# Optimization experiments

Hardware: AMD Instinct MI355X
Metric: run time of the kernel (lower is better)

Reference implementation:

```python
import jax, jax.numpy as jnp
import numpy as np

M = 0.5
S = 64.0
LS_EPS = 0.0
COS_M = float(np.cos(M))
SIN_M = float(np.sin(M))
THRESHOLD = float(np.cos(np.pi - M))
MM = float(np.sin(np.pi - M) * M)
N_CLASSES = 100000


def setup_inputs() -> dict:
    key = jax.random.key(0)
    k1, k2, k3 = jax.random.split(key, 3)
    embeddings = jax.random.normal(k1, (1024, 512), dtype=jnp.float32)
    kernel = jax.random.normal(k2, (512, N_CLASSES), dtype=jnp.float32) * 0.01
    t = jnp.zeros((1,), dtype=jnp.float32)
    label = jax.random.randint(k3, (1024,), 0, N_CLASSES, dtype=jnp.int64)
    return {"embeddings": embeddings, "kernel": kernel, "t": t, "label": label}


def reference(embeddings, kernel, t, label):
    # l2-normalize embeddings over feature axis, kernel over input axis
    emb = embeddings / jnp.linalg.norm(embeddings, axis=1, keepdims=True)
    kn = kernel / jnp.linalg.norm(kernel, axis=0, keepdims=True)
    cos_theta = jnp.clip(emb @ kn, -1.0, 1.0)  # [N, C]
    n = embeddings.shape[0]
    rows = jnp.arange(n)
    target_logit = cos_theta[rows, label][:, None]  # [N, 1]
    sin_theta = jnp.sqrt(1.0 - target_logit ** 2)
    cos_theta_m = target_logit * COS_M - sin_theta * SIN_M  # [N, 1]
    mask = cos_theta > cos_theta_m  # hard examples (broadcast per row)
    final_target_logit = jnp.where(target_logit > THRESHOLD,
                                   cos_theta_m, target_logit - MM)
    # running-mean buffer update (no-grad in original)
    t_new = jax.lax.stop_gradient(target_logit.mean() * 0.01 + 0.99 * t[0])
    cos_theta = jnp.where(mask, cos_theta * (t_new + cos_theta), cos_theta)
    cos_theta = cos_theta.at[rows, label].set(final_target_logit[:, 0])
    if LS_EPS > 0:
        cos_theta = (1 - LS_EPS) * cos_theta + LS_EPS / N_CLASSES
    return cos_theta * S
```

## Files before the change

### kernel.cpp

```cpp
#include <hip/hip_runtime.h>

typedef unsigned short u16;
typedef unsigned int u32;
typedef __attribute__((ext_vector_type(8))) short bf16x8;
typedef __attribute__((ext_vector_type(4))) float f32x4;

#define KDIM   512
#define NROWS  1024
#define NCLS   100000
#define CPAD   100096
#define NSTRIP 782
#define NMT    8

#define COS_M_C   0.8775825618903728f
#define SIN_M_C   0.4794255386042030f
#define THRESH_C  (-0.8775825618903728f)
#define MM_C      0.2397127693021015f
#define S_C       64.0f

__device__ __forceinline__ u16 f2bf(float f) {
    u32 x = __float_as_uint(f);
    x += 0x7fffu + ((x >> 16) & 1u);
    return (u16)(x >> 16);
}
__device__ __forceinline__ float bf2f(u16 u) {
    return __uint_as_float(((u32)u) << 16);
}
__device__ __forceinline__ u32 pack2(float a, float b) {
    return (u32)f2bf(a) | ((u32)f2bf(b) << 16);
}
__device__ __forceinline__ int phi(int r, int q) {
    return r * 4 + ((q + r + (r >> 1)) & 3);
}

__device__ __forceinline__ void gld16(const void* g, void* l) {
    __builtin_amdgcn_global_load_lds(
        (const __attribute__((address_space(1))) void*)g,
        (__attribute__((address_space(3))) void*)l, 16, 0, 0);
}

__global__ __launch_bounds__(64)
void norm_emb_k(const float* __restrict__ emb, float* __restrict__ Af,
                u16* __restrict__ Aw) {
    const int i = blockIdx.x, l = threadIdx.x;
    const float* e = emb + i * KDIM;
    float4 v0 = *(const float4*)(e + l * 8);
    float4 v1 = *(const float4*)(e + l * 8 + 4);
    float s = v0.x*v0.x + v0.y*v0.y + v0.z*v0.z + v0.w*v0.w
            + v1.x*v1.x + v1.y*v1.y + v1.z*v1.z + v1.w*v1.w;
    #pragma unroll
    for (int o = 1; o < 64; o <<= 1) s += __shfl_xor(s, o);
    float inv = rsqrtf(s);
    float4 n0 = make_float4(v0.x*inv, v0.y*inv, v0.z*inv, v0.w*inv);
    float4 n1 = make_float4(v1.x*inv, v1.y*inv, v1.z*inv, v1.w*inv);
    *(float4*)(Af + i*KDIM + l*8)     = n0;
    *(float4*)(Af + i*KDIM + l*8 + 4) = n1;
    const int mt = i >> 7, g = (i >> 4) & 7, r = i & 15;
    const int kc = l >> 2, q = l & 3;
    uint4 w;
    w.x = pack2(n0.x, n0.y);
    w.y = pack2(n0.z, n0.w);
    w.z = pack2(n1.x, n1.y);
    w.w = pack2(n1.z, n1.w);
    *(uint4*)(Aw + mt*65536 + kc*4096 + g*512 + phi(r, q)*8) = w;
}

__global__ __launch_bounds__(128)
void transpose_norm_k(const float* __restrict__ Kg, u16* __restrict__ Bn,
                      float* __restrict__ kinv) {
    __shared__ float Ls[32 * 132];
    const int t  = threadIdx.x;
    const int jb = blockIdx.x * 128;
    const int j  = jb + t;
    u16* bstrip = Bn + (size_t)blockIdx.x * 65536;
    float acc = 0.f;
    for (int kc = 0; kc < 16; ++kc) {
        #pragma unroll
        for (int it = 0; it < 8; ++it) {
            int fid  = it * 128 + t;
            int r    = fid >> 5;
            int c4   = (fid & 31) * 4;
            int gcol = jb + c4;
            float4 v;
            if (gcol + 3 < NCLS) {
                v = *(const float4*)(Kg + (kc*32 + r) * NCLS + gcol);
            } else {
                v.x = (gcol + 0 < NCLS) ? Kg[(kc*32 + r)*NCLS + gcol + 0] : 0.f;
                v.y = (gcol + 1 < NCLS) ? Kg[(kc*32 + r)*NCLS + gcol + 1] : 0.f;
                v.z = (gcol + 2 < NCLS) ? Kg[(kc*32 + r)*NCLS + gcol + 2] : 0.f;
                v.w = (gcol + 3 < NCLS) ? Kg[(kc*32 + r)*NCLS + gcol + 3] : 0.f;
            }
            *(float4*)(Ls + r * 132 + c4) = v;
        }
        __syncthreads();
        #pragma unroll
        for (int q = 0; q < 4; ++q) {
            u16 u[8];
            #pragma unroll
            for (int e = 0; e < 8; ++e) {
                float v = Ls[(q*8 + e) * 132 + t];
                acc += v * v;
                u[e] = f2bf(v);
            }
            uint4 w;
            w.x = (u32)u[0] | ((u32)u[1] << 16);
            w.y = (u32)u[2] | ((u32)u[3] << 16);
            w.z = (u32)u[4] | ((u32)u[5] << 16);
            w.w = (u32)u[6] | ((u32)u[7] << 16);
            *(uint4*)(bstrip + kc*4096 + (t>>4)*512 + phi(t & 15, q)*8) = w;
        }
        __syncthreads();
    }
    kinv[j] = rsqrtf(fmaxf(acc, 1e-30f));
}

__global__ __launch_bounds__(64)
void target_k(const float* __restrict__ Af, const u16* __restrict__ Bn,
              const float* __restrict__ kinv, const int* __restrict__ label,
              float* __restrict__ tgt, float* __restrict__ ctm,
              float* __restrict__ fin) {
    const int i = blockIdx.x, l = threadIdx.x;
    const int lab = label[i];
    const float* a = Af + i * KDIM + l * 8;
    float4 a0 = *(const float4*)a;
    float4 a1 = *(const float4*)(a + 4);
    uint4 bv = *(const uint4*)(Bn + (size_t)(lab >> 7) * 65536
               + (l >> 2) * 4096 + ((lab >> 4) & 7) * 512 + phi(lab & 15, l & 3) * 8);
    float d = a0.x * bf2f((u16)(bv.x & 0xffff)) + a0.y * bf2f((u16)(bv.x >> 16))
            + a0.z * bf2f((u16)(bv.y & 0xffff)) + a0.w * bf2f((u16)(bv.y >> 16))
            + a1.x * bf2f((u16)(bv.z & 0xffff)) + a1.y * bf2f((u16)(bv.z >> 16))
            + a1.z * bf2f((u16)(bv.w & 0xffff)) + a1.w * bf2f((u16)(bv.w >> 16));
    #pragma unroll
    for (int o = 1; o < 64; o <<= 1) d += __shfl_xor(d, o);
    if (l == 0) {
        float c = d * kinv[lab];
        c = fminf(fmaxf(c, -1.f), 1.f);
        tgt[i] = c;
        float sn = sqrtf(fmaxf(1.f - c*c, 0.f));
        float cm = c * COS_M_C - sn * SIN_M_C;
        ctm[i] = cm;
        fin[i] = (c > THRESH_C) ? cm : (c - MM_C);
    }
}

__global__ __launch_bounds__(256)
void tnew_k(const float* __restrict__ tgt, const float* __restrict__ tin,
            float* __restrict__ tnw) {
    __shared__ float red[256];
    const int t = threadIdx.x;
    float s = tgt[t] + tgt[t + 256] + tgt[t + 512] + tgt[t + 768];
    red[t] = s;
    __syncthreads();
    for (int o = 128; o > 0; o >>= 1) {
        if (t < o) red[t] += red[t + o];
        __syncthreads();
    }
    if (t == 0) tnw[0] = red[0] * (0.01f / 1024.f) + 0.99f * tin[0];
}

__global__ __launch_bounds__(256, 4)
void gemm_k(const u16* __restrict__ A, const u16* __restrict__ B,
            const float* __restrict__ kinv, const float* __restrict__ ctm,
            const float* __restrict__ fin, const int* __restrict__ label,
            const float* __restrict__ tnwp, float* __restrict__ out) {
    __shared__ __align__(16) u16 As[2][4096];
    __shared__ __align__(16) u16 Bs[2][4096];
    const int tid  = threadIdx.x;
    const int wave = tid >> 6, lane = tid & 63;

    const int L  = blockIdx.x;
    const int w  = (L & 7) * NSTRIP + (L >> 3);
    const int mt = w & 7;
    const int cs = w >> 3;
    const int m0 = mt * 128;
    const int j0 = cs * 128;
    const int wr = (wave >> 1) * 64;
    const int wc = (wave & 1) * 64;

    f32x4 acc[4][4] = {};

    const u16* gA = A + mt * 65536 + tid * 8;
    const u16* gB = B + (size_t)cs * 65536 + tid * 8;
    const int l0 = tid * 8, l1 = tid * 8 + 2048;

    const int pphi = phi(lane & 15, lane >> 4) * 16;
    const int aG = (wr >> 4) * 1024 + pphi;
    const int bG = (wc >> 4) * 1024 + pphi;

#define STAGE(b, ks) do {                               \
    gld16(gA + (ks) * 4096,        &As[b][l0]);         \
    gld16(gA + (ks) * 4096 + 2048, &As[b][l1]);         \
    gld16(gB + (ks) * 4096,        &Bs[b][l0]);         \
    gld16(gB + (ks) * 4096 + 2048, &Bs[b][l1]);         \
} while (0)

    STAGE(0, 0);
    STAGE(1, 1);
    #pragma unroll
    for (int ks = 0; ks < 16; ++ks) {
        const int cur = ks & 1;
        if (ks < 15) asm volatile("s_waitcnt vmcnt(4)" ::: "memory");
        else         asm volatile("s_waitcnt vmcnt(0)" ::: "memory");
        __builtin_amdgcn_s_barrier();
        __builtin_amdgcn_sched_barrier(0);

        const char* ab = (const char*)As[cur] + aG;
        const char* bb = (const char*)Bs[cur] + bG;
        bf16x8 af[4], bfr[4];
        #pragma unroll
        for (int m = 0; m < 4; ++m)
            af[m] = *(const bf16x8*)(ab + m * 1024);
        #pragma unroll
        for (int n = 0; n < 4; ++n)
            bfr[n] = *(const bf16x8*)(bb + n * 1024);

        asm volatile("s_waitcnt lgkmcnt(0)" ::: "memory");
        __builtin_amdgcn_sched_barrier(0);
        __builtin_amdgcn_s_barrier();
        __builtin_amdgcn_sched_barrier(0);

        if (ks < 14) STAGE(cur, ks + 2);

        __builtin_amdgcn_s_setprio(1);
        #pragma unroll
        for (int m = 0; m < 4; ++m)
            #pragma unroll
            for (int n = 0; n < 4; ++n)
                acc[m][n] = __builtin_amdgcn_mfma_f32_16x16x32_bf16(
                                af[m], bfr[n], acc[m][n], 0, 0, 0);
        __builtin_amdgcn_s_setprio(0);
    }
#undef STAGE

    const float tnew = *tnwp;
    const int colbase = j0 + wc + (lane & 15);
    float kv[4];
    int cols[4];
    #pragma unroll
    for (int n = 0; n < 4; ++n) {
        cols[n] = colbase + n * 16;
        kv[n] = (cols[n] < NCLS) ? kinv[cols[n]] : 0.f;
    }
    #pragma unroll
    for (int m = 0; m < 4; ++m) {
        const int rb = m0 + wr + m * 16 + (lane >> 4) * 4;
        #pragma unroll
        for (int r = 0; r < 4; ++r) {
            const int row = rb + r;
            const int lab = label[row];
            const float ct = ctm[row];
            const float fv = fin[row];
            float* orow = out + (size_t)row * NCLS;
            #pragma unroll
            for (int n = 0; n < 4; ++n) {
                float c = acc[m][n][r] * kv[n];
                c = fminf(fmaxf(c, -1.f), 1.f);
                float v = (c > ct) ? c * (tnew + c) : c;
                v = (cols[n] == lab) ? fv : v;
                if (cols[n] < NCLS)
                    orow[cols[n]] = v * S_C;
            }
        }
    }
}

extern "C" void kernel_launch(void* const* d_in, const int* in_sizes, int n_in,
                              void* d_out, int out_size, void* d_ws, size_t ws_size,
                              hipStream_t stream) {
    const float* emb = (const float*)d_in[0];
    const float* Kg  = (const float*)d_in[1];
    const float* tin = (const float*)d_in[2];
    const int*   lab = (const int*)d_in[3];
    float* out = (float*)d_out;

    char* w = (char*)d_ws;
    u16*   Bn   = (u16*)w;
    u16*   Aw   = (u16*)(w + 102498304);
    float* Af   = (float*)(w + 103546880);
    float* kinv = (float*)(w + 105644032);
    float* tgt  = (float*)(w + 106044416);
    float* ctmv = (float*)(w + 106048512);
    float* finv = (float*)(w + 106052608);
    float* tnw  = (float*)(w + 106056704);

    norm_emb_k<<<NROWS, 64, 0, stream>>>(emb, Af, Aw);
    transpose_norm_k<<<NSTRIP, 128, 0, stream>>>(Kg, Bn, kinv);
    target_k<<<NROWS, 64, 0, stream>>>(Af, Bn, kinv, lab, tgt, ctmv, finv);
    tnew_k<<<1, 256, 0, stream>>>(tgt, tin, tnw);
    gemm_k<<<NSTRIP * NMT, 256, 0, stream>>>(
        Aw, Bn, kinv, ctmv, finv, lab, tnw, out);
}
```

Before: 370.0 us.

## Enlarge GEMM tile to 256x256 with 512 threads and XOR-swizzled 64-K layout

The GEMM block tile grows from 128x128 with 256 threads to 256x256 with 512 threads. Each wave now computes 128x64, and the K step is 64, so there are 8 iterations instead of 16. The packed A/B layouts in the normalization and transpose kernels switch to a row-major 64-wide K chunk with an XOR-style swizzle. The pipeline also prefetches the next stage before waiting, and the XCD-aware block remap is adjusted. The goal is more data reuse per byte loaded and fewer barriers. The cost is higher register and LDS use, 64 KB per block, and lower occupancy.

After: 388.3 us. +4.9%, slower.

```diff
diff --git a/kernel.cpp b/kernel.cpp
--- a/kernel.cpp
+++ b/kernel.cpp
@@ -9,8 +9,9 @@
 #define NROWS  1024
 #define NCLS   100000
 #define CPAD   100096
-#define NSTRIP 782
-#define NMT    8
+#define NSTRIP 391
+#define NMT    4
+#define NWG    (NSTRIP*NMT)
 
 #define COS_M_C   0.8775825618903728f
 #define SIN_M_C   0.4794255386042030f
@@ -29,15 +30,13 @@
 __device__ __forceinline__ u32 pack2(float a, float b) {
     return (u32)f2bf(a) | ((u32)f2bf(b) << 16);
 }
-__device__ __forceinline__ int phi(int r, int q) {
-    return r * 4 + ((q + r + (r >> 1)) & 3);
-}
 
 __device__ __forceinline__ void gld16(const void* g, void* l) {
     __builtin_amdgcn_global_load_lds(
         (const __attribute__((address_space(1))) void*)g,
         (__attribute__((address_space(3))) void*)l, 16, 0, 0);
 }
+
 
 __global__ __launch_bounds__(64)
 void norm_emb_k(const float* __restrict__ emb, float* __restrict__ Af,
@@ -55,31 +54,31 @@
     float4 n1 = make_float4(v1.x*inv, v1.y*inv, v1.z*inv, v1.w*inv);
     *(float4*)(Af + i*KDIM + l*8)     = n0;
     *(float4*)(Af + i*KDIM + l*8 + 4) = n1;
-    const int mt = i >> 7, g = (i >> 4) & 7, r = i & 15;
-    const int kc = l >> 2, q = l & 3;
+    const int mt = i >> 8, row = i & 255;
     uint4 w;
     w.x = pack2(n0.x, n0.y);
     w.y = pack2(n0.z, n0.w);
     w.z = pack2(n1.x, n1.y);
     w.w = pack2(n1.z, n1.w);
-    *(uint4*)(Aw + mt*65536 + kc*4096 + g*512 + phi(r, q)*8) = w;
-}
-
-__global__ __launch_bounds__(128)
+    *(uint4*)(Aw + mt*131072 + (l>>3)*16384 + row*64
+              + (((l&7) + row) & 7) * 8) = w;
+}
+
+__global__ __launch_bounds__(256)
 void transpose_norm_k(const float* __restrict__ Kg, u16* __restrict__ Bn,
                       float* __restrict__ kinv) {
-    __shared__ float Ls[32 * 132];
+    __shared__ float Ls[32 * 260];
     const int t  = threadIdx.x;
-    const int jb = blockIdx.x * 128;
+    const int jb = blockIdx.x * 256;
     const int j  = jb + t;
-    u16* bstrip = Bn + (size_t)blockIdx.x * 65536;
+    u16* bstrip = Bn + (size_t)blockIdx.x * 131072;
     float acc = 0.f;
     for (int kc = 0; kc < 16; ++kc) {
         #pragma unroll
         for (int it = 0; it < 8; ++it) {
-            int fid  = it * 128 + t;
-            int r    = fid >> 5;
-            int c4   = (fid & 31) * 4;
+            int fid  = it * 256 + t;
+            int r    = fid >> 6;
+            int c4   = (fid & 63) * 4;
             int gcol = jb + c4;
             float4 v;
             if (gcol + 3 < NCLS) {
@@ -90,15 +89,15 @@
                 v.z = (gcol + 2 < NCLS) ? Kg[(kc*32 + r)*NCLS + gcol + 2] : 0.f;
                 v.w = (gcol + 3 < NCLS) ? Kg[(kc*32 + r)*NCLS + gcol + 3] : 0.f;
             }
-            *(float4*)(Ls + r * 132 + c4) = v;
+            *(float4*)(Ls + r * 260 + c4) = v;
         }
         __syncthreads();
         #pragma unroll
-        for (int q = 0; q < 4; ++q) {
+        for (int sub = 0; sub < 4; ++sub) {
             u16 u[8];
             #pragma unroll
             for (int e = 0; e < 8; ++e) {
-                float v = Ls[(q*8 + e) * 132 + t];
+                float v = Ls[(sub*8 + e) * 260 + t];
                 acc += v * v;
                 u[e] = f2bf(v);
             }
@@ -107,7 +106,8 @@
             w.y = (u32)u[2] | ((u32)u[3] << 16);
             w.z = (u32)u[4] | ((u32)u[5] << 16);
             w.w = (u32)u[6] | ((u32)u[7] << 16);
-            *(uint4*)(bstrip + kc*4096 + (t>>4)*512 + phi(t & 15, q)*8) = w;
+            *(uint4*)(bstrip + (kc>>1)*16384 + t*64
+                      + ((((kc&1)*4 + sub) + t) & 7) * 8) = w;
         }
         __syncthreads();
     }
@@ -121,11 +121,12 @@
               float* __restrict__ fin) {
     const int i = blockIdx.x, l = threadIdx.x;
     const int lab = label[i];
-    const float* a = Af + i * KDIM + l * 8;
-    float4 a0 = *(const float4*)a;
-    float4 a1 = *(const float4*)(a + 4);
-    uint4 bv = *(const uint4*)(Bn + (size_t)(lab >> 7) * 65536
-               + (l >> 2) * 4096 + ((lab >> 4) & 7) * 512 + phi(lab & 15, l & 3) * 8);
+    const int kbase = (l >> 3) * 64 + (l & 7) * 8;
+    float4 a0 = *(const float4*)(Af + i * KDIM + kbase);
+    float4 a1 = *(const float4*)(Af + i * KDIM + kbase + 4);
+    const int col = lab & 255;
+    uint4 bv = *(const uint4*)(Bn + (size_t)(lab >> 8) * 131072
+               + (l >> 3) * 16384 + col * 64 + (((l & 7) + col) & 7) * 8);
     float d = a0.x * bf2f((u16)(bv.x & 0xffff)) + a0.y * bf2f((u16)(bv.x >> 16))
             + a0.z * bf2f((u16)(bv.y & 0xffff)) + a0.w * bf2f((u16)(bv.y >> 16))
             + a1.x * bf2f((u16)(bv.z & 0xffff)) + a1.y * bf2f((u16)(bv.z >> 16))
@@ -158,92 +159,118 @@
     if (t == 0) tnw[0] = red[0] * (0.01f / 1024.f) + 0.99f * tin[0];
 }
 
-__global__ __launch_bounds__(256, 4)
+__global__ __launch_bounds__(512, 2)
 void gemm_k(const u16* __restrict__ A, const u16* __restrict__ B,
             const float* __restrict__ kinv, const float* __restrict__ ctm,
             const float* __restrict__ fin, const int* __restrict__ label,
             const float* __restrict__ tnwp, float* __restrict__ out) {
-    __shared__ __align__(16) u16 As[2][4096];
-    __shared__ __align__(16) u16 Bs[2][4096];
+    __shared__ __align__(16) u16 As[2][16384];
+    __shared__ __align__(16) u16 Bs[2][16384];
     const int tid  = threadIdx.x;
     const int wave = tid >> 6, lane = tid & 63;
 
-    const int L  = blockIdx.x;
-    const int w  = (L & 7) * NSTRIP + (L >> 3);
-    const int mt = w & 7;
-    const int cs = w >> 3;
-    const int m0 = mt * 128;
-    const int j0 = cs * 128;
-    const int wr = (wave >> 1) * 64;
-    const int wc = (wave & 1) * 64;
-
-    f32x4 acc[4][4] = {};
-
-    const u16* gA = A + mt * 65536 + tid * 8;
-    const u16* gB = B + (size_t)cs * 65536 + tid * 8;
-    const int l0 = tid * 8, l1 = tid * 8 + 2048;
-
-    const int pphi = phi(lane & 15, lane >> 4) * 16;
-    const int aG = (wr >> 4) * 1024 + pphi;
-    const int bG = (wc >> 4) * 1024 + pphi;
-
-#define STAGE(b, ks) do {                               \
-    gld16(gA + (ks) * 4096,        &As[b][l0]);         \
-    gld16(gA + (ks) * 4096 + 2048, &As[b][l1]);         \
-    gld16(gB + (ks) * 4096,        &Bs[b][l0]);         \
-    gld16(gB + (ks) * 4096 + 2048, &Bs[b][l1]);         \
+    const int L   = blockIdx.x;
+    const int xcd = L & 7;
+    const int wg  = (xcd < 4 ? xcd * 196 : 784 + (xcd - 4) * 195) + (L >> 3);
+    const int mt  = wg & 3;
+    const int cs  = wg >> 2;
+    const int m0  = mt * 256;
+    const int j0  = cs * 256;
+    const int wrl = (wave >> 2) * 128;
+    const int wcl = (wave & 3) * 64;
+
+    f32x4 acc[8][4] = {};
+
+    const u16* gA = A + mt * 131072 + tid * 8;
+    const u16* gB = B + (size_t)cs * 131072 + tid * 8;
+    const int  ld = tid * 8;
+
+    const int rowA = wrl + (lane & 15);
+    const int colB = wcl + (lane & 15);
+    const int qh   = lane >> 4;
+    const int aOff0 = rowA * 64 + ((qh     + rowA) & 7) * 8;
+    const int aOff1 = rowA * 64 + ((qh + 4 + rowA) & 7) * 8;
+    const int bOff0 = colB * 64 + ((qh     + colB) & 7) * 8;
+    const int bOff1 = colB * 64 + ((qh + 4 + colB) & 7) * 8;
+
+#define STAGE(b, kt) do {                                        \
+    gld16(gA + (kt)*16384 +     0, &As[b][ld]);                  \
+    gld16(gA + (kt)*16384 +  4096, &As[b][ld + 4096]);           \
+    gld16(gA + (kt)*16384 +  8192, &As[b][ld + 8192]);           \
+    gld16(gA + (kt)*16384 + 12288, &As[b][ld + 12288]);          \
+    gld16(gB + (kt)*16384 +     0, &Bs[b][ld]);                  \
+    gld16(gB + (kt)*16384 +  4096, &Bs[b][ld + 4096]);           \
+    gld16(gB + (kt)*16384 +  8192, &Bs[b][ld + 8192]);           \
+    gld16(gB + (kt)*16384 + 12288, &Bs[b][ld + 12288]);          \
 } while (0)
 
     STAGE(0, 0);
-    STAGE(1, 1);
-    #pragma unroll
-    for (int ks = 0; ks < 16; ++ks) {
-        const int cur = ks & 1;
-        if (ks < 15) asm volatile("s_waitcnt vmcnt(4)" ::: "memory");
-        else         asm volatile("s_waitcnt vmcnt(0)" ::: "memory");
+    #pragma unroll 2
+    for (int kt = 0; kt < 8; ++kt) {
+        const int cur = kt & 1;
+        if (kt < 7) {
+            STAGE(cur ^ 1, kt + 1);
+            asm volatile("s_waitcnt vmcnt(8)" ::: "memory");
+        } else {
+            asm volatile("s_waitcnt vmcnt(0)" ::: "memory");
+        }
         __builtin_amdgcn_s_barrier();
         __builtin_amdgcn_sched_barrier(0);
 
-        const char* ab = (const char*)As[cur] + aG;
-        const char* bb = (const char*)Bs[cur] + bG;
-        bf16x8 af[4], bfr[4];
-        #pragma unroll
-        for (int m = 0; m < 4; ++m)
-            af[m] = *(const bf16x8*)(ab + m * 1024);
+        const u16* a = As[cur];
+        const u16* b = Bs[cur];
+        bf16x8 af[8], bfr[4];
+
+        #pragma unroll
+        for (int m = 0; m < 8; ++m)
+            af[m] = *(const bf16x8*)(a + aOff0 + m * 1024);
         #pragma unroll
         for (int n = 0; n < 4; ++n)
-            bfr[n] = *(const bf16x8*)(bb + n * 1024);
-
+            bfr[n] = *(const bf16x8*)(b + bOff0 + n * 1024);
         asm volatile("s_waitcnt lgkmcnt(0)" ::: "memory");
         __builtin_amdgcn_sched_barrier(0);
-        __builtin_amdgcn_s_barrier();
-        __builtin_amdgcn_sched_barrier(0);
-
-        if (ks < 14) STAGE(cur, ks + 2);
-
         __builtin_amdgcn_s_setprio(1);
         #pragma unroll
-        for (int m = 0; m < 4; ++m)
+        for (int m = 0; m < 8; ++m)
             #pragma unroll
             for (int n = 0; n < 4; ++n)
                 acc[m][n] = __builtin_amdgcn_mfma_f32_16x16x32_bf16(
                                 af[m], bfr[n], acc[m][n], 0, 0, 0);
         __builtin_amdgcn_s_setprio(0);
+
+        #pragma unroll
+        for (int m = 0; m < 8; ++m)
+            af[m] = *(const bf16x8*)(a + aOff1 + m * 1024);
+        #pragma unroll
+        for (int n = 0; n < 4; ++n)
+            bfr[n] = *(const bf16x8*)(b + bOff1 + n * 1024);
+        asm volatile("s_waitcnt lgkmcnt(0)" ::: "memory");
+        __builtin_amdgcn_sched_barrier(0);
+        __builtin_amdgcn_s_barrier();
+        __builtin_amdgcn_sched_barrier(0);
+        __builtin_amdgcn_s_setprio(1);
+        #pragma unroll
+        for (int m = 0; m < 8; ++m)
+            #pragma unroll
+            for (int n = 0; n < 4; ++n)
+                acc[m][n] = __builtin_amdgcn_mfma_f32_16x16x32_bf16(
+                                af[m], bfr[n], acc[m][n], 0, 0, 0);
+        __builtin_amdgcn_s_setprio(0);
     }
 #undef STAGE
 
     const float tnew = *tnwp;
-    const int colbase = j0 + wc + (lane & 15);
+    const int colbase = j0 + wcl + (lane & 15);
     float kv[4];
     int cols[4];
     #pragma unroll
     for (int n = 0; n < 4; ++n) {
         cols[n] = colbase + n * 16;
-        kv[n] = (cols[n] < NCLS) ? kinv[cols[n]] : 0.f;
+        kv[n] = kinv[cols[n]];
     }
     #pragma unroll
-    for (int m = 0; m < 4; ++m) {
-        const int rb = m0 + wr + m * 16 + (lane >> 4) * 4;
+    for (int m = 0; m < 8; ++m) {
+        const int rb = m0 + wrl + m * 16 + (lane >> 4) * 4;
         #pragma unroll
         for (int r = 0; r < 4; ++r) {
             const int row = rb + r;
@@ -284,9 +311,9 @@
     float* tnw  = (float*)(w + 106056704);
 
     norm_emb_k<<<NROWS, 64, 0, stream>>>(emb, Af, Aw);
-    transpose_norm_k<<<NSTRIP, 128, 0, stream>>>(Kg, Bn, kinv);
+    transpose_norm_k<<<NSTRIP, 256, 0, stream>>>(Kg, Bn, kinv);
     target_k<<<NROWS, 64, 0, stream>>>(Af, Bn, kinv, lab, tgt, ctmv, finv);
     tnew_k<<<1, 256, 0, stream>>>(tgt, tin, tnw);
-    gemm_k<<<NSTRIP * NMT, 256, 0, stream>>>(
+    gemm_k<<<NWG, 512, 0, stream>>>(
         Aw, Bn, kinv, ctmv, finv, lab, tnw, out);
 }
```

## Switch LDS tile layout to row-major swizzle and restructure GEMM prefetch loop

Applied to the files above, without the earlier changes.

Replaces the grouped phi-swizzled LDS/workspace layout with a simpler row-major 32-element-per-row layout using a psi XOR-style swizzle, updated consistently in the producer kernels, target_k, and the GEMM fragment loads. The GEMM main loop now prefetches one stage ahead, issued at the top of each iteration, instead of two stages ahead after the fragment reads. It also drops the s_setprio hints and the kinv bounds check. The aim is simpler addressing and fewer bank conflicts, but the shallower prefetch may expose more memory latency, and the kinv reads for padded columns rely on that workspace being readable.

Result: no change. 368.7 us (-0.4%).

```diff
diff --git a/kernel.cpp b/kernel.cpp
--- a/kernel.cpp
+++ b/kernel.cpp
@@ -11,6 +11,7 @@
 #define CPAD   100096
 #define NSTRIP 782
 #define NMT    8
+#define NWG    (NSTRIP*NMT)
 
 #define COS_M_C   0.8775825618903728f
 #define SIN_M_C   0.4794255386042030f
@@ -29,8 +30,8 @@
 __device__ __forceinline__ u32 pack2(float a, float b) {
     return (u32)f2bf(a) | ((u32)f2bf(b) << 16);
 }
-__device__ __forceinline__ int phi(int r, int q) {
-    return r * 4 + ((q + r + (r >> 1)) & 3);
+__device__ __forceinline__ int psi(int q, int r) {
+    return (q + r + (r >> 2)) & 3;
 }
 
 __device__ __forceinline__ void gld16(const void* g, void* l) {
@@ -38,6 +39,7 @@
         (const __attribute__((address_space(1))) void*)g,
         (__attribute__((address_space(3))) void*)l, 16, 0, 0);
 }
+
 
 __global__ __launch_bounds__(64)
 void norm_emb_k(const float* __restrict__ emb, float* __restrict__ Af,
@@ -55,14 +57,14 @@
     float4 n1 = make_float4(v1.x*inv, v1.y*inv, v1.z*inv, v1.w*inv);
     *(float4*)(Af + i*KDIM + l*8)     = n0;
     *(float4*)(Af + i*KDIM + l*8 + 4) = n1;
-    const int mt = i >> 7, g = (i >> 4) & 7, r = i & 15;
-    const int kc = l >> 2, q = l & 3;
+    const int mt = i >> 7, row = i & 127;
     uint4 w;
     w.x = pack2(n0.x, n0.y);
     w.y = pack2(n0.z, n0.w);
     w.z = pack2(n1.x, n1.y);
     w.w = pack2(n1.z, n1.w);
-    *(uint4*)(Aw + mt*65536 + kc*4096 + g*512 + phi(r, q)*8) = w;
+    *(uint4*)(Aw + mt*65536 + (l>>2)*4096 + row*32
+              + psi(l & 3, row) * 8) = w;
 }
 
 __global__ __launch_bounds__(128)
@@ -107,7 +109,7 @@
             w.y = (u32)u[2] | ((u32)u[3] << 16);
             w.z = (u32)u[4] | ((u32)u[5] << 16);
             w.w = (u32)u[6] | ((u32)u[7] << 16);
-            *(uint4*)(bstrip + kc*4096 + (t>>4)*512 + phi(t & 15, q)*8) = w;
+            *(uint4*)(bstrip + kc*4096 + t*32 + psi(q, t) * 8) = w;
         }
         __syncthreads();
     }
@@ -121,11 +123,11 @@
               float* __restrict__ fin) {
     const int i = blockIdx.x, l = threadIdx.x;
     const int lab = label[i];
-    const float* a = Af + i * KDIM + l * 8;
-    float4 a0 = *(const float4*)a;
-    float4 a1 = *(const float4*)(a + 4);
+    float4 a0 = *(const float4*)(Af + i * KDIM + l * 8);
+    float4 a1 = *(const float4*)(Af + i * KDIM + l * 8 + 4);
+    const int col = lab & 127;
     uint4 bv = *(const uint4*)(Bn + (size_t)(lab >> 7) * 65536
-               + (l >> 2) * 4096 + ((lab >> 4) & 7) * 512 + phi(lab & 15, l & 3) * 8);
+               + (l >> 2) * 4096 + col * 32 + psi(l & 3, col) * 8);
     float d = a0.x * bf2f((u16)(bv.x & 0xffff)) + a0.y * bf2f((u16)(bv.x >> 16))
             + a0.z * bf2f((u16)(bv.y & 0xffff)) + a0.w * bf2f((u16)(bv.y >> 16))
             + a1.x * bf2f((u16)(bv.z & 0xffff)) + a1.y * bf2f((u16)(bv.z >> 16))
@@ -181,54 +183,50 @@
 
     const u16* gA = A + mt * 65536 + tid * 8;
     const u16* gB = B + (size_t)cs * 65536 + tid * 8;
-    const int l0 = tid * 8, l1 = tid * 8 + 2048;
-
-    const int pphi = phi(lane & 15, lane >> 4) * 16;
-    const int aG = (wr >> 4) * 1024 + pphi;
-    const int bG = (wc >> 4) * 1024 + pphi;
-
-#define STAGE(b, ks) do {                               \
-    gld16(gA + (ks) * 4096,        &As[b][l0]);         \
-    gld16(gA + (ks) * 4096 + 2048, &As[b][l1]);         \
-    gld16(gB + (ks) * 4096,        &Bs[b][l0]);         \
-    gld16(gB + (ks) * 4096 + 2048, &Bs[b][l1]);         \
+    const int  ld = tid * 8;
+
+    const int rowA = wr + (lane & 15);
+    const int colB = wc + (lane & 15);
+    const int qh   = lane >> 4;
+    const int aBase = rowA * 32 + psi(qh, rowA) * 8;
+    const int bBase = colB * 32 + psi(qh, colB) * 8;
+
+#define STAGE(b, kt) do {                                        \
+    gld16(gA + (kt)*4096,        &As[b][ld]);                    \
+    gld16(gA + (kt)*4096 + 2048, &As[b][ld + 2048]);             \
+    gld16(gB + (kt)*4096,        &Bs[b][ld]);                    \
+    gld16(gB + (kt)*4096 + 2048, &Bs[b][ld + 2048]);             \
 } while (0)
 
     STAGE(0, 0);
-    STAGE(1, 1);
-    #pragma unroll
-    for (int ks = 0; ks < 16; ++ks) {
-        const int cur = ks & 1;
-        if (ks < 15) asm volatile("s_waitcnt vmcnt(4)" ::: "memory");
-        else         asm volatile("s_waitcnt vmcnt(0)" ::: "memory");
+    #pragma unroll 2
+    for (int kt = 0; kt < 16; ++kt) {
+        const int cur = kt & 1;
+        if (kt < 15) {
+            STAGE(cur ^ 1, kt + 1);
+            asm volatile("s_waitcnt vmcnt(4)" ::: "memory");
+        } else {
+            asm volatile("s_waitcnt vmcnt(0)" ::: "memory");
+        }
         __builtin_amdgcn_s_barrier();
-        __builtin_amdgcn_sched_barrier(0);
-
-        const char* ab = (const char*)As[cur] + aG;
-        const char* bb = (const char*)Bs[cur] + bG;
+
         bf16x8 af[4], bfr[4];
         #pragma unroll
         for (int m = 0; m < 4; ++m)
-            af[m] = *(const bf16x8*)(ab + m * 1024);
+            af[m] = *(const bf16x8*)(As[cur] + aBase + m * 512);
         #pragma unroll
         for (int n = 0; n < 4; ++n)
-            bfr[n] = *(const bf16x8*)(bb + n * 1024);
-
+            bfr[n] = *(const bf16x8*)(Bs[cur] + bBase + n * 512);
         asm volatile("s_waitcnt lgkmcnt(0)" ::: "memory");
         __builtin_amdgcn_sched_barrier(0);
         __builtin_amdgcn_s_barrier();
-        __builtin_amdgcn_sched_barrier(0);
-
-        if (ks < 14) STAGE(cur, ks + 2);
-
-        __builtin_amdgcn_s_setprio(1);
+
         #pragma unroll
         for (int m = 0; m < 4; ++m)
             #pragma unroll
             for (int n = 0; n < 4; ++n)
                 acc[m][n] = __builtin_amdgcn_mfma_f32_16x16x32_bf16(
                                 af[m], bfr[n], acc[m][n], 0, 0, 0);
-        __builtin_amdgcn_s_setprio(0);
     }
 #undef STAGE
 
@@ -239,7 +237,7 @@
     #pragma unroll
     for (int n = 0; n < 4; ++n) {
         cols[n] = colbase + n * 16;
-        kv[n] = (cols[n] < NCLS) ? kinv[cols[n]] : 0.f;
+        kv[n] = kinv[cols[n]];
     }
     #pragma unroll
     for (int m = 0; m < 4; ++m) {
@@ -287,6 +285,6 @@
     transpose_norm_k<<<NSTRIP, 128, 0, stream>>>(Kg, Bn, kinv);
     target_k<<<NROWS, 64, 0, stream>>>(Af, Bn, kinv, lab, tgt, ctmv, finv);
     tnew_k<<<1, 256, 0, stream>>>(tgt, tin, tnw);
-    gemm_k<<<NSTRIP * NMT, 256, 0, stream>>>(
+    gemm_k<<<NWG, 256, 0, stream>>>(
         Aw, Bn, kinv, ctmv, finv, lab, tnw, out);
 }
```
